# Performance work log

Hardware: AMD Instinct MI355X
Metric: run time of the kernel (lower is better)

Reference implementation:

```python
import jax, jax.numpy as jnp
import numpy as np

IN_DIM, H1, H2, N_CLASSES = 128, 100, 128, 19
BATCH, SEQ = 512, 256


def _lstm_relu(x, W, U, b, units):
    """Keras LSTM with activation='relu', recurrent_activation='sigmoid'.
    x: [B, T, D]. Returns (all hidden states [B, T, units], last hidden [B, units]).
    Gate order (Keras): i, f, g(cell candidate), o.
    """
    B = x.shape[0]
    h0 = jnp.zeros((B, units), x.dtype)
    c0 = jnp.zeros((B, units), x.dtype)

    # precompute input projections for all timesteps: [T, B, 4*units]
    zx = jnp.einsum('btd,dk->tbk', x, W) + b

    def step(carry, zx_t):
        h, c = carry
        z = zx_t + h @ U
        i, f, g, o = jnp.split(z, 4, axis=-1)
        i = jax.nn.sigmoid(i)
        f = jax.nn.sigmoid(f)
        g = jax.nn.relu(g)          # activation='relu'
        o = jax.nn.sigmoid(o)
        c = f * c + i * g
        h = o * jax.nn.relu(c)      # output activation is also relu
        return (h, c), h

    (h_last, _), hs = jax.lax.scan(step, (h0, c0), zx)
    return jnp.transpose(hs, (1, 0, 2)), h_last


def setup_inputs() -> dict:
    key = jax.random.key(0)
    ks = jax.random.split(key, 9)
    def w(k, shape, fan_in):
        return jax.random.normal(k, shape, jnp.float32) / np.sqrt(fan_in)
    x = jax.random.normal(ks[0], (BATCH, SEQ, IN_DIM), jnp.float32)
    return {
        'x': x,
        'W1': w(ks[1], (IN_DIM, 4 * H1), IN_DIM),
        'U1': w(ks[2], (H1, 4 * H1), H1),
        'b1': jnp.zeros((4 * H1,), jnp.float32),
        'W2': w(ks[3], (H1, 4 * H2), H1),
        'U2': w(ks[4], (H2, 4 * H2), H2),
        'b2': jnp.zeros((4 * H2,), jnp.float32),
        'Wd': w(ks[5], (H2, N_CLASSES), H2),
        'bd': jnp.zeros((N_CLASSES,), jnp.float32),
    }


def reference(x, W1, U1, b1, W2, U2, b2, Wd, bd):
    h1_seq, _ = _lstm_relu(x, W1, U1, b1, H1)      # [B, T, 100]
    _, h2 = _lstm_relu(h1_seq, W2, U2, b2, H2)     # [B, 128] (last step only)
    logits = h2 @ Wd + bd
    return jax.nn.softmax(logits, axis=-1)         # [B, 19]
```

## Files before the change

kernel.cpp:

```cpp
#include <hip/hip_runtime.h>
#include <math.h>


#define T_SEQ 256
#define BATCH 512
#define IN_DIM 128
#define H1 100
#define H2 128
#define NCLS 19

typedef float f4v __attribute__((ext_vector_type(4)));
typedef short s8v __attribute__((ext_vector_type(8)));

#define FOR_GA(M) M(0) M(1) M(2) M(3)

__device__ __forceinline__ void lds_barrier_() {
    __asm__ volatile("s_waitcnt lgkmcnt(0)\n\ts_barrier" ::: "memory");
}

__device__ __forceinline__ float sigmoidf_(float x) {
    return 1.0f / (1.0f + __expf(-x));
}
__device__ __forceinline__ f4v sig4_(f4v z) {
    f4v r;
    r.x = sigmoidf_(z.x); r.y = sigmoidf_(z.y);
    r.z = sigmoidf_(z.z); r.w = sigmoidf_(z.w);
    return r;
}
__device__ __forceinline__ f4v relu4_(f4v z) {
    f4v r;
    r.x = fmaxf(z.x, 0.f); r.y = fmaxf(z.y, 0.f);
    r.z = fmaxf(z.z, 0.f); r.w = fmaxf(z.w, 0.f);
    return r;
}
__device__ __forceinline__ short bf_hi_(float x, float& hif) {
    unsigned u = __builtin_bit_cast(unsigned, x);
    unsigned r = (u + 0x7FFFu + ((u >> 16) & 1u)) & 0xFFFF0000u;
    hif = __builtin_bit_cast(float, r);
    return (short)(r >> 16);
}
__device__ __forceinline__ void bsplit_(float x, short& hi, short& lo) {
    float hif;
    hi = bf_hi_(x, hif);
    float rs = x - hif;
    float d;
    lo = bf_hi_(rs, d);
}
__device__ __forceinline__ float bf2f_(short s) {
    unsigned v = ((unsigned)(unsigned short)s) << 16;
    return __builtin_bit_cast(float, v);
}
template<bool PAD>
__device__ __forceinline__ void load_bf_(const float* __restrict__ U,
                                         int u, int ga, int kt, int lq,
                                         s8v& hi, s8v& lo) {
    short h, l;
#pragma unroll
    for (int j = 0; j < 8; ++j) {
        int k = kt * 32 + lq * 8 + j;
        float x;
        if (PAD) x = (u < 100 && k < 100) ? U[(size_t)k * 400 + ga * 100 + u] : 0.0f;
        else     x = U[(size_t)k * 512 + ga * 128 + u];
        bsplit_(x, h, l);
        hi[j] = h; lo[j] = l;
    }
}

template<bool PAD, bool SEQOUT, bool INIT, bool WROUT>
__global__ __launch_bounds__(512)
__attribute__((amdgpu_waves_per_eu(1, 2)))
void recg_kernel(const float* __restrict__ zx,
                 const float* __restrict__ U,
                 float* __restrict__ outp,
                 float* __restrict__ cbuf,
                 float* __restrict__ hbuf,
                 int tlen)
{
    constexpr int HLD = 136;
    constexpr int HSZ = 16 * HLD;
    __shared__ __align__(16) short hsH[2][HSZ];
    __shared__ __align__(16) short hsL[2][HSZ];

    const int tid = threadIdx.x;
    const int wv = tid >> 6;
    const int lane = tid & 63;
    const int lm = lane & 15;
    const int lq = lane >> 4;
    const int u = 16 * wv + lm;
    const int blk16 = blockIdx.x * 16;

#define BDECL(ga) \
    s8v bh##ga##_0, bl##ga##_0, bh##ga##_1, bl##ga##_1, \
        bh##ga##_2, bl##ga##_2, bh##ga##_3, bl##ga##_3; \
    load_bf_<PAD>(U, u, ga, 0, lq, bh##ga##_0, bl##ga##_0); \
    load_bf_<PAD>(U, u, ga, 1, lq, bh##ga##_1, bl##ga##_1); \
    load_bf_<PAD>(U, u, ga, 2, lq, bh##ga##_2, bl##ga##_2); \
    load_bf_<PAD>(U, u, ga, 3, lq, bh##ga##_3, bl##ga##_3);
    FOR_GA(BDECL)
#undef BDECL

    if (INIT) {
        for (int i = tid; i < HSZ; i += 512) { hsH[0][i] = 0; hsL[0][i] = 0; }
    } else {
        int row = tid >> 5, c4 = (tid & 31) * 4;
        f4v hvv = *(const f4v*)&hbuf[(size_t)(blk16 + row) * 128 + c4];
        short hb, lb;
        bsplit_(hvv.x, hb, lb); hsH[0][row * HLD + c4 + 0] = hb; hsL[0][row * HLD + c4 + 0] = lb;
        bsplit_(hvv.y, hb, lb); hsH[0][row * HLD + c4 + 1] = hb; hsL[0][row * HLD + c4 + 1] = lb;
        bsplit_(hvv.z, hb, lb); hsH[0][row * HLD + c4 + 2] = hb; hsL[0][row * HLD + c4 + 2] = lb;
        bsplit_(hvv.w, hb, lb); hsH[0][row * HLD + c4 + 3] = hb; hsL[0][row * HLD + c4 + 3] = lb;
    }
    f4v cst = {0.f, 0.f, 0.f, 0.f};
    if (!INIT) {
        const float* pc = cbuf + (size_t)(blk16 + lq * 4) * 128 + u;
        cst = (f4v){pc[0], pc[128], pc[256], pc[384]};
    }
    f4v zc0, zc1, zc2, zc3, zn0, zn1, zn2, zn3;
#define ZLD(ga, tt, dst) { \
    const float* p = zx + ((size_t)(tt) * BATCH + blk16 + lq * 4) * 512 + (ga) * 128 + u; \
    dst##ga = (f4v){p[0], p[512], p[1024], p[1536]}; }
    ZLD(0, 0, zc) ZLD(1, 0, zc) ZLD(2, 0, zc) ZLD(3, 0, zc)
    __syncthreads();

#define MKT(kt) { \
    const s8v ah = *(const s8v*)&hsH[cur][lm * HLD + (kt) * 32 + lq * 8]; \
    const s8v al = *(const s8v*)&hsL[cur][lm * HLD + (kt) * 32 + lq * 8]; \
    ac0 = __builtin_amdgcn_mfma_f32_16x16x32_bf16(ah, bh0_##kt, ac0, 0, 0, 0); \
    ac0 = __builtin_amdgcn_mfma_f32_16x16x32_bf16(al, bh0_##kt, ac0, 0, 0, 0); \
    ac0 = __builtin_amdgcn_mfma_f32_16x16x32_bf16(ah, bl0_##kt, ac0, 0, 0, 0); \
    ac1 = __builtin_amdgcn_mfma_f32_16x16x32_bf16(ah, bh1_##kt, ac1, 0, 0, 0); \
    ac1 = __builtin_amdgcn_mfma_f32_16x16x32_bf16(al, bh1_##kt, ac1, 0, 0, 0); \
    ac1 = __builtin_amdgcn_mfma_f32_16x16x32_bf16(ah, bl1_##kt, ac1, 0, 0, 0); \
    ac2 = __builtin_amdgcn_mfma_f32_16x16x32_bf16(ah, bh2_##kt, ac2, 0, 0, 0); \
    ac2 = __builtin_amdgcn_mfma_f32_16x16x32_bf16(al, bh2_##kt, ac2, 0, 0, 0); \
    ac2 = __builtin_amdgcn_mfma_f32_16x16x32_bf16(ah, bl2_##kt, ac2, 0, 0, 0); \
    ac3 = __builtin_amdgcn_mfma_f32_16x16x32_bf16(ah, bh3_##kt, ac3, 0, 0, 0); \
    ac3 = __builtin_amdgcn_mfma_f32_16x16x32_bf16(al, bh3_##kt, ac3, 0, 0, 0); \
    ac3 = __builtin_amdgcn_mfma_f32_16x16x32_bf16(ah, bl3_##kt, ac3, 0, 0, 0); }

#pragma unroll 1
    for (int t = 0; t < tlen; ++t) {
        const int cur = t & 1, nxt = cur ^ 1;
        int tn = (t + 1 < tlen) ? t + 1 : t;
        ZLD(0, tn, zn) ZLD(1, tn, zn) ZLD(2, tn, zn) ZLD(3, tn, zn)
        f4v ac0 = zc0, ac1 = zc1, ac2 = zc2, ac3 = zc3;
        MKT(0) MKT(1) MKT(2) MKT(3)
        f4v iv = sig4_(ac0), fv = sig4_(ac1), gv = relu4_(ac2), ov = sig4_(ac3);
        cst = fv * cst + iv * gv;
        f4v hv = ov * relu4_(cst);
        short hb, lb;
        bsplit_(hv.x, hb, lb); hsH[nxt][(lq * 4 + 0) * HLD + u] = hb; hsL[nxt][(lq * 4 + 0) * HLD + u] = lb;
        bsplit_(hv.y, hb, lb); hsH[nxt][(lq * 4 + 1) * HLD + u] = hb; hsL[nxt][(lq * 4 + 1) * HLD + u] = lb;
        bsplit_(hv.z, hb, lb); hsH[nxt][(lq * 4 + 2) * HLD + u] = hb; hsL[nxt][(lq * 4 + 2) * HLD + u] = lb;
        bsplit_(hv.w, hb, lb); hsH[nxt][(lq * 4 + 3) * HLD + u] = hb; hsL[nxt][(lq * 4 + 3) * HLD + u] = lb;
        if (SEQOUT) {
            if (!PAD || u < 100) {
                float* po = outp + ((size_t)t * BATCH + blk16 + lq * 4) * 100 + u;
                po[0] = hv.x; po[100] = hv.y; po[200] = hv.z; po[300] = hv.w;
            }
        }
        lds_barrier_();
        zc0 = zn0; zc1 = zn1; zc2 = zn2; zc3 = zn3;
    }
#undef MKT
#undef ZLD

    const int fin = tlen & 1;
    {
        int row = tid >> 5, c4 = (tid & 31) * 4;
        f4v hvv;
        hvv.x = bf2f_(hsH[fin][row * HLD + c4 + 0]) + bf2f_(hsL[fin][row * HLD + c4 + 0]);
        hvv.y = bf2f_(hsH[fin][row * HLD + c4 + 1]) + bf2f_(hsL[fin][row * HLD + c4 + 1]);
        hvv.z = bf2f_(hsH[fin][row * HLD + c4 + 2]) + bf2f_(hsL[fin][row * HLD + c4 + 2]);
        hvv.w = bf2f_(hsH[fin][row * HLD + c4 + 3]) + bf2f_(hsL[fin][row * HLD + c4 + 3]);
        *(f4v*)&hbuf[(size_t)(blk16 + row) * 128 + c4] = hvv;
        if (WROUT) *(f4v*)&outp[(size_t)(blk16 + row) * 128 + c4] = hvv;
    }
    {
        float* pc = cbuf + (size_t)(blk16 + lq * 4) * 128 + u;
        pc[0] = cst.x; pc[128] = cst.y; pc[256] = cst.z; pc[384] = cst.w;
    }
}

__global__ __launch_bounds__(256, 2)
void proj1p_kernel(const float* __restrict__ x, const float* __restrict__ W1,
                   const float* __restrict__ b1, float* __restrict__ out, int t0)
{
    constexpr int LD = 132;
    __shared__ __align__(16) float As[32 * LD];
    __shared__ __align__(16) float Ws[32 * LD];
    const int tid = threadIdx.x;
    const int b = blockIdx.x;
    const int c0 = blockIdx.y * 128;
    const int ty = tid >> 4, tx = tid & 15;
    const float* A = x + ((size_t)b * T_SEQ + t0) * IN_DIM;

#define PACC(i) f4v accL##i = {0.f,0.f,0.f,0.f}; f4v accR##i = {0.f,0.f,0.f,0.f};
    PACC(0) PACC(1) PACC(2) PACC(3) PACC(4) PACC(5) PACC(6) PACC(7)
#undef PACC

    for (int kk = 0; kk < IN_DIM; kk += 32) {
        __syncthreads();
#pragma unroll
        for (int i = 0; i < 4; ++i) {
            int idx = tid + i * 256;
            int row = idx >> 3, kg = idx & 7;
            int k = kk + kg * 4;
            f4v v = *(const f4v*)&A[(size_t)row * IN_DIM + k];
            As[(kg * 4 + 0) * LD + row] = v.x;
            As[(kg * 4 + 1) * LD + row] = v.y;
            As[(kg * 4 + 2) * LD + row] = v.z;
            As[(kg * 4 + 3) * LD + row] = v.w;
        }
#pragma unroll
        for (int i = 0; i < 4; ++i) {
            int idx = tid + i * 256;
            int k = idx >> 5, cg = idx & 31;
            int gk = kk + k;
            int gcp = c0 + cg * 4;
            int gate = gcp >> 7, ub = gcp & 127;
            f4v v;
            v.x = (ub + 0 < 100) ? W1[(size_t)gk * 400 + gate * 100 + ub + 0] : 0.f;
            v.y = (ub + 1 < 100) ? W1[(size_t)gk * 400 + gate * 100 + ub + 1] : 0.f;
            v.z = (ub + 2 < 100) ? W1[(size_t)gk * 400 + gate * 100 + ub + 2] : 0.f;
            v.w = (ub + 3 < 100) ? W1[(size_t)gk * 400 + gate * 100 + ub + 3] : 0.f;
            *(f4v*)&Ws[k * LD + cg * 4] = v;
        }
        __syncthreads();
#pragma unroll
        for (int k = 0; k < 32; ++k) {
            f4v av0 = *(const f4v*)&As[k * LD + ty * 8];
            f4v av1 = *(const f4v*)&As[k * LD + ty * 8 + 4];
            f4v b0v = *(const f4v*)&Ws[k * LD + tx * 8];
            f4v b1v = *(const f4v*)&Ws[k * LD + tx * 8 + 4];
#define PFMA(i, s) accL##i += (s) * b0v; accR##i += (s) * b1v;
            PFMA(0, av0.x) PFMA(1, av0.y) PFMA(2, av0.z) PFMA(3, av0.w)
            PFMA(4, av1.x) PFMA(5, av1.y) PFMA(6, av1.z) PFMA(7, av1.w)
#undef PFMA
        }
    }

    const int cb = c0 + tx * 8;
    f4v bL, bR;
#pragma unroll
    for (int j = 0; j < 4; ++j) {
        int gate = (cb + j) >> 7, uu = (cb + j) & 127;
        bL[j] = (uu < 100) ? b1[gate * 100 + uu] : 0.f;
    }
#pragma unroll
    for (int j = 0; j < 4; ++j) {
        int gate = (cb + 4 + j) >> 7, uu = (cb + 4 + j) & 127;
        bR[j] = (uu < 100) ? b1[gate * 100 + uu] : 0.f;
    }
#define PST(i) { \
        int tl = ty * 8 + i; \
        size_t orow = (size_t)tl * BATCH + b; \
        f4v vL = accL##i + bL; *(f4v*)&out[orow * 512 + cb] = vL; \
        f4v vR = accR##i + bR; *(f4v*)&out[orow * 512 + cb + 4] = vR; }
    PST(0) PST(1) PST(2) PST(3) PST(4) PST(5) PST(6) PST(7)
#undef PST
}

#define PREP8(M)  M(0) M(1) M(2) M(3) M(4) M(5) M(6) M(7)
template<int K, int N, bool SWAP>
__global__ __launch_bounds__(256, 2)
void proj_kernel(const float* __restrict__ A, const float* __restrict__ W,
                 const float* __restrict__ bias, float* __restrict__ out)
{
    constexpr int LD = 132;
    __shared__ __align__(16) float As[32 * LD];
    __shared__ __align__(16) float Ws[32 * LD];
    const int tid = threadIdx.x;
    const int r0 = blockIdx.x * 128;
    const int c0 = blockIdx.y * 128;
    const int ty = tid >> 4, tx = tid & 15;

#define PACC(i) f4v accL##i = {0.f,0.f,0.f,0.f}; f4v accR##i = {0.f,0.f,0.f,0.f};
    PREP8(PACC)
#undef PACC

    for (int kk = 0; kk < K; kk += 32) {
        __syncthreads();
#pragma unroll
        for (int i = 0; i < 4; ++i) {
            int idx = tid + i * 256;
            int row = idx >> 3, kg = idx & 7;
            int k = kk + kg * 4;
            f4v v = {0.f, 0.f, 0.f, 0.f};
            if (k < K) v = *(const f4v*)&A[(size_t)(r0 + row) * K + k];
            As[(kg * 4 + 0) * LD + row] = v.x;
            As[(kg * 4 + 1) * LD + row] = v.y;
            As[(kg * 4 + 2) * LD + row] = v.z;
            As[(kg * 4 + 3) * LD + row] = v.w;
        }
#pragma unroll
        for (int i = 0; i < 4; ++i) {
            int idx = tid + i * 256;
            int k = idx >> 5, cg = idx & 31;
            int gk = kk + k, gc = c0 + cg * 4;
            f4v v = {0.f, 0.f, 0.f, 0.f};
            if (gk < K && gc < N) v = *(const f4v*)&W[(size_t)gk * N + gc];
            *(f4v*)&Ws[k * LD + cg * 4] = v;
        }
        __syncthreads();
#pragma unroll
        for (int k = 0; k < 32; ++k) {
            f4v av0 = *(const f4v*)&As[k * LD + ty * 8];
            f4v av1 = *(const f4v*)&As[k * LD + ty * 8 + 4];
            f4v b0v = *(const f4v*)&Ws[k * LD + tx * 8];
            f4v b1v = *(const f4v*)&Ws[k * LD + tx * 8 + 4];
#define PFMA(i, s) accL##i += (s) * b0v; accR##i += (s) * b1v;
            PFMA(0, av0.x) PFMA(1, av0.y) PFMA(2, av0.z) PFMA(3, av0.w)
            PFMA(4, av1.x) PFMA(5, av1.y) PFMA(6, av1.z) PFMA(7, av1.w)
#undef PFMA
        }
    }

    const int cb = c0 + tx * 8;
    f4v bL, bR;
#pragma unroll
    for (int j = 0; j < 4; ++j) bL[j] = (cb + j < N) ? bias[cb + j] : 0.f;
#pragma unroll
    for (int j = 0; j < 4; ++j) bR[j] = (cb + 4 + j < N) ? bias[cb + 4 + j] : 0.f;
#define PST(i) { \
        int r = r0 + ty * 8 + i; \
        size_t orow = SWAP ? ((size_t)(r & 255) * BATCH + (r >> 8)) : (size_t)r; \
        if (cb < N)     { f4v v = accL##i + bL; *(f4v*)&out[orow * N + cb] = v; } \
        if (cb + 4 < N) { f4v v = accR##i + bR; *(f4v*)&out[orow * N + cb + 4] = v; } }
    PREP8(PST)
#undef PST
}

__global__ __launch_bounds__(64, 1)
void dense_softmax_kernel(const float* __restrict__ h2, const float* __restrict__ Wd,
                          const float* __restrict__ bd, float* __restrict__ out)
{
    const int b = blockIdx.x;
    const int k = threadIdx.x;
    __shared__ __align__(16) float hsm[H2];
    if (k < H2 / 4) ((f4v*)hsm)[k] = ((const f4v*)(h2 + (size_t)b * H2))[k];
    __syncthreads();

    float logit = -1e30f;
    if (k < NCLS) {
        float acc = bd[k];
#pragma unroll
        for (int d = 0; d < H2; ++d) acc += hsm[d] * Wd[d * NCLS + k];
        logit = acc;
    }
    float m = logit;
#pragma unroll
    for (int off = 32; off >= 1; off >>= 1) m = fmaxf(m, __shfl_xor(m, off, 64));
    float e = (k < NCLS) ? __expf(logit - m) : 0.0f;
    float s = e;
#pragma unroll
    for (int off = 32; off >= 1; off >>= 1) s += __shfl_xor(s, off, 64);
    if (k < NCLS) out[(size_t)b * NCLS + k] = e / s;
}

__global__ __launch_bounds__(448, 1)
void lstm1_fb(const float* __restrict__ x, const float* __restrict__ W1,
              const float* __restrict__ U1, const float* __restrict__ b1,
              float* __restrict__ h1out)
{
    const int b = blockIdx.x;
    const int k = threadIdx.x;
    __shared__ __align__(16) float xs[IN_DIM];
    __shared__ __align__(16) float hs[H1];
    __shared__ __align__(16) float zs[4 * H1];
    float w1r[IN_DIM];
    float u1r[H1];
    float bias = 0.0f;
    if (k < 4 * H1) {
        bias = b1[k];
#pragma unroll
        for (int d = 0; d < IN_DIM; ++d) w1r[d] = W1[d * (4 * H1) + k];
#pragma unroll
        for (int j = 0; j < H1; ++j) u1r[j] = U1[j * (4 * H1) + k];
    }
    if (k < H1) hs[k] = 0.0f;
    if (k < IN_DIM / 4)
        ((float4*)xs)[k] = ((const float4*)(x + ((size_t)b * T_SEQ) * IN_DIM))[k];
    float c = 0.0f;
    __syncthreads();
    for (int t = 0; t < T_SEQ; ++t) {
        if (k < 4 * H1) {
            float acc0 = bias, acc1 = 0.f, acc2 = 0.f, acc3 = 0.f;
#pragma unroll
            for (int q = 0; q < IN_DIM / 4; ++q) {
                float4 xv = ((const float4*)xs)[q];
                acc0 += xv.x * w1r[4 * q]; acc1 += xv.y * w1r[4 * q + 1];
                acc2 += xv.z * w1r[4 * q + 2]; acc3 += xv.w * w1r[4 * q + 3];
            }
#pragma unroll
            for (int q = 0; q < H1 / 4; ++q) {
                float4 hv = ((const float4*)hs)[q];
                acc0 += hv.x * u1r[4 * q]; acc1 += hv.y * u1r[4 * q + 1];
                acc2 += hv.z * u1r[4 * q + 2]; acc3 += hv.w * u1r[4 * q + 3];
            }
            float zv = (acc0 + acc1) + (acc2 + acc3);
            zs[k] = (k >= 2 * H1 && k < 3 * H1) ? fmaxf(zv, 0.0f) : sigmoidf_(zv);
        }
        __syncthreads();
        if (k < H1) {
            float i = zs[k], f = zs[k + H1], g = zs[k + 2 * H1], o = zs[k + 3 * H1];
            c = f * c + i * g;
            float h = o * fmaxf(c, 0.0f);
            hs[k] = h;
            h1out[((size_t)t * BATCH + b) * H1 + k] = h;
        }
        int tn = t + 1;
        if (tn < T_SEQ && k < IN_DIM / 4)
            ((float4*)xs)[k] = ((const float4*)(x + ((size_t)b * T_SEQ + tn) * IN_DIM))[k];
        __syncthreads();
    }
}

__global__ __launch_bounds__(512, 1)
void lstm2_fb(const float* __restrict__ h1in, const float* __restrict__ W2,
              const float* __restrict__ U2, const float* __restrict__ b2,
              float* __restrict__ h2out)
{
    const int b = blockIdx.x;
    const int k = threadIdx.x;
    __shared__ __align__(16) float ps[H1];
    __shared__ __align__(16) float hs[H2];
    __shared__ __align__(16) float zs[4 * H2];
    float w2r[H1];
    float u2r[H2];
    float bias = b2[k];
#pragma unroll
    for (int j = 0; j < H1; ++j) w2r[j] = W2[j * (4 * H2) + k];
#pragma unroll
    for (int j = 0; j < H2; ++j) u2r[j] = U2[j * (4 * H2) + k];
    if (k < H2) hs[k] = 0.0f;
    if (k < H1 / 4)
        ((float4*)ps)[k] = ((const float4*)(h1in + (size_t)b * H1))[k];
    float c = 0.0f;
    float hlast = 0.0f;
    __syncthreads();
    for (int t = 0; t < T_SEQ; ++t) {
        float acc0 = bias, acc1 = 0.f, acc2 = 0.f, acc3 = 0.f;
#pragma unroll
        for (int q = 0; q < H1 / 4; ++q) {
            float4 pv = ((const float4*)ps)[q];
            acc0 += pv.x * w2r[4 * q]; acc1 += pv.y * w2r[4 * q + 1];
            acc2 += pv.z * w2r[4 * q + 2]; acc3 += pv.w * w2r[4 * q + 3];
        }
#pragma unroll
        for (int q = 0; q < H2 / 4; ++q) {
            float4 hv = ((const float4*)hs)[q];
            acc0 += hv.x * u2r[4 * q]; acc1 += hv.y * u2r[4 * q + 1];
            acc2 += hv.z * u2r[4 * q + 2]; acc3 += hv.w * u2r[4 * q + 3];
        }
        float zv = (acc0 + acc1) + (acc2 + acc3);
        zs[k] = (k >= 2 * H2 && k < 3 * H2) ? fmaxf(zv, 0.0f) : sigmoidf_(zv);
        __syncthreads();
        if (k < H2) {
            float i = zs[k], f = zs[k + H2], g = zs[k + 2 * H2], o = zs[k + 3 * H2];
            c = f * c + i * g;
            hlast = o * fmaxf(c, 0.0f);
            hs[k] = hlast;
        }
        int tn = t + 1;
        if (tn < T_SEQ && k < H1 / 4)
            ((float4*)ps)[k] = ((const float4*)(h1in + ((size_t)tn * BATCH + b) * H1))[k];
        __syncthreads();
    }
    if (k < H2) h2out[(size_t)b * H2 + k] = hlast;
}

extern "C" void kernel_launch(void* const* d_in, const int* in_sizes, int n_in,
                              void* d_out, int out_size, void* d_ws, size_t ws_size,
                              hipStream_t stream) {
    const float* x  = (const float*)d_in[0];
    const float* W1 = (const float*)d_in[1];
    const float* U1 = (const float*)d_in[2];
    const float* b1 = (const float*)d_in[3];
    const float* W2 = (const float*)d_in[4];
    const float* U2 = (const float*)d_in[5];
    const float* b2 = (const float*)d_in[6];
    const float* Wd = (const float*)d_in[7];
    const float* bd = (const float*)d_in[8];
    float* out = (float*)d_out;

    const int TC = T_SEQ / 2;
    const size_t zx_elems = (size_t)TC * BATCH * 512;
    const size_t h1_elems = (size_t)T_SEQ * BATCH * H1;
    const size_t st_elems = (size_t)BATCH * H2;
    const size_t need = (zx_elems + h1_elems + 5 * st_elems) * sizeof(float);

    if (ws_size >= need) {
        float* zxbuf = (float*)d_ws;
        float* h1buf = zxbuf + zx_elems;
        float* c1buf = h1buf + h1_elems;
        float* hc1buf = c1buf + st_elems;
        float* c2buf = hc1buf + st_elems;
        float* hc2buf = c2buf + st_elems;
        float* h2buf = hc2buf + st_elems;

        hipLaunchKernelGGL(proj1p_kernel, dim3(BATCH, 4), dim3(256), 0, stream,
                           x, W1, b1, zxbuf, 0);
        hipLaunchKernelGGL((recg_kernel<true, true, true, false>), dim3(32), dim3(512), 0, stream,
                           zxbuf, U1, h1buf, c1buf, hc1buf, TC);
        hipLaunchKernelGGL(proj1p_kernel, dim3(BATCH, 4), dim3(256), 0, stream,
                           x, W1, b1, zxbuf, TC);
        hipLaunchKernelGGL((recg_kernel<true, true, false, false>), dim3(32), dim3(512), 0, stream,
                           zxbuf, U1, h1buf + (size_t)TC * BATCH * H1, c1buf, hc1buf, TC);
        hipLaunchKernelGGL((proj_kernel<H1, 4 * H2, false>), dim3(512, 4), dim3(256), 0, stream,
                           h1buf, W2, b2, zxbuf);
        hipLaunchKernelGGL((recg_kernel<false, false, true, false>), dim3(32), dim3(512), 0, stream,
                           zxbuf, U2, (float*)nullptr, c2buf, hc2buf, TC);
        hipLaunchKernelGGL((proj_kernel<H1, 4 * H2, false>), dim3(512, 4), dim3(256), 0, stream,
                           h1buf + (size_t)TC * BATCH * H1, W2, b2, zxbuf);
        hipLaunchKernelGGL((recg_kernel<false, false, false, true>), dim3(32), dim3(512), 0, stream,
                           zxbuf, U2, h2buf, c2buf, hc2buf, TC);

        hipLaunchKernelGGL(dense_softmax_kernel, dim3(BATCH), dim3(64), 0, stream,
                           h2buf, Wd, bd, out);
    } else {
        float* h1buf = (float*)d_ws;
        float* h2buf = h1buf + h1_elems;
        hipLaunchKernelGGL(lstm1_fb, dim3(BATCH), dim3(448), 0, stream, x, W1, U1, b1, h1buf);
        hipLaunchKernelGGL(lstm2_fb, dim3(BATCH), dim3(512), 0, stream, h1buf, W2, U2, b2, h2buf);
        hipLaunchKernelGGL(dense_softmax_kernel, dim3(BATCH), dim3(64), 0, stream, h2buf, Wd, bd, out);
    }
}
```

Measured before the change: 1.372 ms.

## Split recurrent kernel over 128 blocks of 4 batch rows each

The recurrent LSTM kernel now handles 4 batch rows per block instead of 16 and launches 128 blocks instead of 32, so more CUs work on the sequential recurrence at once. The MFMA tile is still 16 rows wide, so 12 of the 16 rows are zero padding. Only the lq==0 lanes load zx, update state and write h. This spreads the latency-bound time loop across more CUs, but each MFMA now does only a quarter of useful work and U is loaded into registers by four times as many blocks.

```diff
diff --git a/kernel.cpp b/kernel.cpp
--- a/kernel.cpp
+++ b/kernel.cpp
@@ -87,7 +87,7 @@
     const int lm = lane & 15;
     const int lq = lane >> 4;
     const int u = 16 * wv + lm;
-    const int blk16 = blockIdx.x * 16;
+    const int blk4 = blockIdx.x * 4;
 
 #define BDECL(ga) \
     s8v bh##ga##_0, bl##ga##_0, bh##ga##_1, bl##ga##_1, \
@@ -99,25 +99,33 @@
     FOR_GA(BDECL)
 #undef BDECL
 
-    if (INIT) {
-        for (int i = tid; i < HSZ; i += 512) { hsH[0][i] = 0; hsL[0][i] = 0; }
-    } else {
-        int row = tid >> 5, c4 = (tid & 31) * 4;
-        f4v hvv = *(const f4v*)&hbuf[(size_t)(blk16 + row) * 128 + c4];
-        short hb, lb;
-        bsplit_(hvv.x, hb, lb); hsH[0][row * HLD + c4 + 0] = hb; hsL[0][row * HLD + c4 + 0] = lb;
-        bsplit_(hvv.y, hb, lb); hsH[0][row * HLD + c4 + 1] = hb; hsL[0][row * HLD + c4 + 1] = lb;
-        bsplit_(hvv.z, hb, lb); hsH[0][row * HLD + c4 + 2] = hb; hsL[0][row * HLD + c4 + 2] = lb;
-        bsplit_(hvv.w, hb, lb); hsH[0][row * HLD + c4 + 3] = hb; hsL[0][row * HLD + c4 + 3] = lb;
+    for (int i = tid; i < HSZ; i += 512) {
+        hsH[0][i] = 0; hsL[0][i] = 0;
+        hsH[1][i] = 0; hsL[1][i] = 0;
+    }
+    __syncthreads();
+    if (!INIT) {
+        if (tid < 128) {
+            int row = tid >> 5, c4 = (tid & 31) * 4;
+            f4v hvv = *(const f4v*)&hbuf[(size_t)(blk4 + row) * 128 + c4];
+            short hb, lb;
+            bsplit_(hvv.x, hb, lb); hsH[0][row * HLD + c4 + 0] = hb; hsL[0][row * HLD + c4 + 0] = lb;
+            bsplit_(hvv.y, hb, lb); hsH[0][row * HLD + c4 + 1] = hb; hsL[0][row * HLD + c4 + 1] = lb;
+            bsplit_(hvv.z, hb, lb); hsH[0][row * HLD + c4 + 2] = hb; hsL[0][row * HLD + c4 + 2] = lb;
+            bsplit_(hvv.w, hb, lb); hsH[0][row * HLD + c4 + 3] = hb; hsL[0][row * HLD + c4 + 3] = lb;
+        }
     }
     f4v cst = {0.f, 0.f, 0.f, 0.f};
-    if (!INIT) {
-        const float* pc = cbuf + (size_t)(blk16 + lq * 4) * 128 + u;
+    if (!INIT && lq == 0) {
+        const float* pc = cbuf + (size_t)blk4 * 128 + u;
         cst = (f4v){pc[0], pc[128], pc[256], pc[384]};
     }
-    f4v zc0, zc1, zc2, zc3, zn0, zn1, zn2, zn3;
-#define ZLD(ga, tt, dst) { \
-    const float* p = zx + ((size_t)(tt) * BATCH + blk16 + lq * 4) * 512 + (ga) * 128 + u; \
+    f4v zc0 = {0.f,0.f,0.f,0.f}, zc1 = {0.f,0.f,0.f,0.f},
+        zc2 = {0.f,0.f,0.f,0.f}, zc3 = {0.f,0.f,0.f,0.f};
+    f4v zn0 = {0.f,0.f,0.f,0.f}, zn1 = {0.f,0.f,0.f,0.f},
+        zn2 = {0.f,0.f,0.f,0.f}, zn3 = {0.f,0.f,0.f,0.f};
+#define ZLD(ga, tt, dst) if (lq == 0) { \
+    const float* p = zx + ((size_t)(tt) * BATCH + blk4) * 512 + (ga) * 128 + u; \
     dst##ga = (f4v){p[0], p[512], p[1024], p[1536]}; }
     ZLD(0, 0, zc) ZLD(1, 0, zc) ZLD(2, 0, zc) ZLD(3, 0, zc)
     __syncthreads();
@@ -148,15 +156,17 @@
         f4v iv = sig4_(ac0), fv = sig4_(ac1), gv = relu4_(ac2), ov = sig4_(ac3);
         cst = fv * cst + iv * gv;
         f4v hv = ov * relu4_(cst);
-        short hb, lb;
-        bsplit_(hv.x, hb, lb); hsH[nxt][(lq * 4 + 0) * HLD + u] = hb; hsL[nxt][(lq * 4 + 0) * HLD + u] = lb;
-        bsplit_(hv.y, hb, lb); hsH[nxt][(lq * 4 + 1) * HLD + u] = hb; hsL[nxt][(lq * 4 + 1) * HLD + u] = lb;
-        bsplit_(hv.z, hb, lb); hsH[nxt][(lq * 4 + 2) * HLD + u] = hb; hsL[nxt][(lq * 4 + 2) * HLD + u] = lb;
-        bsplit_(hv.w, hb, lb); hsH[nxt][(lq * 4 + 3) * HLD + u] = hb; hsL[nxt][(lq * 4 + 3) * HLD + u] = lb;
-        if (SEQOUT) {
-            if (!PAD || u < 100) {
-                float* po = outp + ((size_t)t * BATCH + blk16 + lq * 4) * 100 + u;
-                po[0] = hv.x; po[100] = hv.y; po[200] = hv.z; po[300] = hv.w;
+        if (lq == 0) {
+            short hb, lb;
+            bsplit_(hv.x, hb, lb); hsH[nxt][0 * HLD + u] = hb; hsL[nxt][0 * HLD + u] = lb;
+            bsplit_(hv.y, hb, lb); hsH[nxt][1 * HLD + u] = hb; hsL[nxt][1 * HLD + u] = lb;
+            bsplit_(hv.z, hb, lb); hsH[nxt][2 * HLD + u] = hb; hsL[nxt][2 * HLD + u] = lb;
+            bsplit_(hv.w, hb, lb); hsH[nxt][3 * HLD + u] = hb; hsL[nxt][3 * HLD + u] = lb;
+            if (SEQOUT) {
+                if (!PAD || u < 100) {
+                    float* po = outp + ((size_t)t * BATCH + blk4) * 100 + u;
+                    po[0] = hv.x; po[100] = hv.y; po[200] = hv.z; po[300] = hv.w;
+                }
             }
         }
         lds_barrier_();
@@ -166,18 +176,18 @@
 #undef ZLD
 
     const int fin = tlen & 1;
-    {
+    if (tid < 128) {
         int row = tid >> 5, c4 = (tid & 31) * 4;
         f4v hvv;
         hvv.x = bf2f_(hsH[fin][row * HLD + c4 + 0]) + bf2f_(hsL[fin][row * HLD + c4 + 0]);
         hvv.y = bf2f_(hsH[fin][row * HLD + c4 + 1]) + bf2f_(hsL[fin][row * HLD + c4 + 1]);
         hvv.z = bf2f_(hsH[fin][row * HLD + c4 + 2]) + bf2f_(hsL[fin][row * HLD + c4 + 2]);
         hvv.w = bf2f_(hsH[fin][row * HLD + c4 + 3]) + bf2f_(hsL[fin][row * HLD + c4 + 3]);
-        *(f4v*)&hbuf[(size_t)(blk16 + row) * 128 + c4] = hvv;
-        if (WROUT) *(f4v*)&outp[(size_t)(blk16 + row) * 128 + c4] = hvv;
-    }
-    {
-        float* pc = cbuf + (size_t)(blk16 + lq * 4) * 128 + u;
+        *(f4v*)&hbuf[(size_t)(blk4 + row) * 128 + c4] = hvv;
+        if (WROUT) *(f4v*)&outp[(size_t)(blk4 + row) * 128 + c4] = hvv;
+    }
+    if (lq == 0) {
+        float* pc = cbuf + (size_t)blk4 * 128 + u;
         pc[0] = cst.x; pc[128] = cst.y; pc[256] = cst.z; pc[384] = cst.w;
     }
 }
@@ -501,19 +511,19 @@
 
         hipLaunchKernelGGL(proj1p_kernel, dim3(BATCH, 4), dim3(256), 0, stream,
                            x, W1, b1, zxbuf, 0);
-        hipLaunchKernelGGL((recg_kernel<true, true, true, false>), dim3(32), dim3(512), 0, stream,
+        hipLaunchKernelGGL((recg_kernel<true, true, true, false>), dim3(128), dim3(512), 0, stream,
                            zxbuf, U1, h1buf, c1buf, hc1buf, TC);
         hipLaunchKernelGGL(proj1p_kernel, dim3(BATCH, 4), dim3(256), 0, stream,
                            x, W1, b1, zxbuf, TC);
-        hipLaunchKernelGGL((recg_kernel<true, true, false, false>), dim3(32), dim3(512), 0, stream,
+        hipLaunchKernelGGL((recg_kernel<true, true, false, false>), dim3(128), dim3(512), 0, stream,
                            zxbuf, U1, h1buf + (size_t)TC * BATCH * H1, c1buf, hc1buf, TC);
         hipLaunchKernelGGL((proj_kernel<H1, 4 * H2, false>), dim3(512, 4), dim3(256), 0, stream,
                            h1buf, W2, b2, zxbuf);
-        hipLaunchKernelGGL((recg_kernel<false, false, true, false>), dim3(32), dim3(512), 0, stream,
+        hipLaunchKernelGGL((recg_kernel<false, false, true, false>), dim3(128), dim3(512), 0, stream,
                            zxbuf, U2, (float*)nullptr, c2buf, hc2buf, TC);
         hipLaunchKernelGGL((proj_kernel<H1, 4 * H2, false>), dim3(512, 4), dim3(256), 0, stream,
                            h1buf + (size_t)TC * BATCH * H1, W2, b2, zxbuf);
-        hipLaunchKernelGGL((recg_kernel<false, false, false, true>), dim3(32), dim3(512), 0, stream,
+        hipLaunchKernelGGL((recg_kernel<false, false, false, true>), dim3(128), dim3(512), 0, stream,
                            zxbuf, U2, h2buf, c2buf, hc2buf, TC);
 
         hipLaunchKernelGGL(dense_softmax_kernel, dim3(BATCH), dim3(64), 0, stream,
```

New measurement: 1.513 ms. 10.2% more time.
